# Optimization experiments

Hardware: AMD Instinct MI355X
Metric: run time of the kernel (lower is better)

Reference implementation:

```python
import jax, jax.numpy as jnp
import numpy as np

K = 40        # nearest neighbors
BN_EPS = 1e-5  # nn.BatchNorm1d default eps


def _bn(x, g, b):
    # training-mode BatchNorm1d: batch mean, biased variance
    mu = x.mean(0)
    var = x.var(0)
    return g * (x - mu) / jnp.sqrt(var + BN_EPS) + b


def setup_inputs() -> dict:
    key = jax.random.key(0)
    ks = jax.random.split(key, 16)
    N, Cin, D, S, P = 8192, 16, 32, 3, 32

    def w(k, i, o):
        return jax.random.normal(k, (i, o), jnp.float32) * (1.0 / np.sqrt(i))

    return {
        "x": jax.random.normal(ks[0], (N, Cin), jnp.float32),
        "original_coords": jax.random.normal(ks[1], (N, 3), jnp.float32),
        "batch": jnp.zeros((N,), jnp.int32),
        "step_count": 0,
        "num_layer": 1,
        # pre_gravnet MLP
        "pre_w1": w(ks[2], Cin, D), "pre_b1": jnp.zeros((D,), jnp.float32),
        "pre_w2": w(ks[3], D, D), "pre_b2": jnp.zeros((D,), jnp.float32),
        "bn1_g": jnp.ones((D,), jnp.float32), "bn1_b": jnp.zeros((D,), jnp.float32),
        # GravNetConv projections
        "lin_s_w": w(ks[4], D, S),
        "lin_h_w": w(ks[5], D, P), "lin_h_b": jnp.zeros((P,), jnp.float32),
        "lin_w": w(ks[6], D + 2 * P, D), "lin_b": jnp.zeros((D,), jnp.float32),
        # post_gravnet MLP (in = out_channels + space_dims + d_shape = 32+3+32)
        "post_w1": w(ks[7], D + S + D, D), "post_b1": jnp.zeros((D,), jnp.float32),
        "post_w2": w(ks[8], D, D), "post_b2": jnp.zeros((D,), jnp.float32),
        "bn2_g": jnp.ones((D,), jnp.float32), "bn2_b": jnp.zeros((D,), jnp.float32),
    }


def reference(x, original_coords, batch, step_count, num_layer,
              pre_w1, pre_b1, pre_w2, pre_b2, bn1_g, bn1_b,
              lin_s_w, lin_h_w, lin_h_b, lin_w, lin_b,
              post_w1, post_b1, post_w2, post_b2, bn2_g, bn2_b):
    N = x.shape[0]

    # pre_gravnet MLP + batchnorm
    h = jax.nn.elu(x @ pre_w1 + pre_b1)
    h = jax.nn.elu(h @ pre_w2 + pre_b2)
    x_in = _bn(h, bn1_g, bn1_b)

    # GravNetConv projections
    h_l = x_in @ lin_h_w + lin_h_b          # [N, P] propagated features
    s_l = x_in @ lin_s_w                    # [N, S] learned coordinate space

    # kNN graph in s-space (self loops excluded)
    sq = jnp.sum(s_l * s_l, axis=1)
    d2 = sq[:, None] + sq[None, :] - 2.0 * (s_l @ s_l.T)   # [N, N]
    d2 = jnp.maximum(d2, 0.0)
    d2 = jnp.where(jnp.eye(N, dtype=bool), jnp.inf, d2)
    _, idx = jax.lax.top_k(-d2, K)           # [N, K] neighbor indices

    # per-edge squared distance (NOTE: propagate uses the SQUARED distance,
    # faithful to the source where edge_weight is never re-bound to sqrt)
    edge_sq = jnp.take_along_axis(d2, idx, axis=1)    # [N, K]
    dist = jnp.sqrt(edge_sq + 1e-6)                   # [N, K]

    # DGL-side reductions at dst = edge_index[1] = neighbor index
    dst = idx.reshape(-1)
    distf = dist.reshape(-1)
    indeg = jax.ops.segment_sum(jnp.ones_like(distf), dst, num_segments=N)
    sum_d = jax.ops.segment_sum(distf, dst, num_segments=N)
    avdist = jnp.where(indeg > 0, sum_d / jnp.maximum(indeg, 1.0), 0.0)
    loss_regularizing_neig = 0.01 * jnp.mean(jnp.square(avdist - 0.5))

    norm_d = distf / (sum_d + 1e-4)[dst]              # EdgeWeightNorm('right')
    # faithful to source bug: '_edge_w_gndist' is set to the NORMALIZED dist,
    # and apply_edges multiplies by the RAW '_edge_w'
    degs2 = jax.ops.segment_sum(norm_d, dst, num_segments=N) + 1e-4
    gn_final = distf / degs2[dst]
    loss_llregulariser = 0.1 * jnp.mean(jnp.square(norm_d - gn_final))

    # message passing: msg = h_l[neighbor] * squared_dist, mean+max over the
    # K neighbors of each source node (regular fan-in -> dense reduce)
    msgs = h_l[idx] * edge_sq[..., None]              # [N, K, P]
    agg = jnp.concatenate([msgs.mean(1), msgs.max(1)], axis=-1)  # [N, 2P]
    xgn = jnp.concatenate([agg, x_in], axis=-1) @ lin_w + lin_b   # [N, 32]

    # post_gravnet MLP + batchnorm
    cat = jnp.concatenate([xgn, s_l, x_in], axis=1)   # [N, 67]
    o = jax.nn.elu(cat @ post_w1 + post_b1)
    o = jax.nn.elu(o @ post_w2 + post_b2)
    out = _bn(o, bn2_g, bn2_b)
    return (out, loss_regularizing_neig, loss_llregulariser)
```

## Files before the change

### kernel.cpp

```cpp
#include <hip/hip_runtime.h>
#include <math.h>

#define NPTS 8192
#define KNN 40
#define DD 32
#define CIN 16
#define RPB 8
#define QT 1024
#define NQTR (NPTS / QT)
#define KQPB 16
#define CAP 96

#define OFF_H      0u
#define OFF_XIN    262144u
#define OFF_HL     524288u
#define OFF_SL     786432u
#define OFF_ESQ    819200u
#define OFF_O      1146880u
#define OFF_IDX    1409024u
#define OFF_SUMD   1736704u
#define OFF_INDEG  1744896u
#define OFF_STATS  1753088u
#define ZERO_FLOATS (8192u + 8192u + 130u * 32u)

#define ST(i) stats[(i) * 32]

__device__ __forceinline__ float elu_f(float x) { return x > 0.f ? x : (expf(x) - 1.f); }

__device__ __forceinline__ float grp_sum32(float v) {
#pragma unroll
    for (int m = 1; m < 32; m <<= 1) v += __shfl_xor(v, m);
    return v;
}

__device__ __forceinline__ float rfl(float v) {
    return __int_as_float(__builtin_amdgcn_readfirstlane(__float_as_int(v)));
}

__device__ __forceinline__ unsigned fkey(float x) {
    unsigned b = __float_as_uint(x);
    return b ^ ((unsigned)((int)b >> 31) | 0x80000000u);
}
__device__ __forceinline__ float kinv(unsigned k) {
    unsigned b = (k & 0x80000000u) ? (k ^ 0x80000000u) : ~k;
    return __uint_as_float(b);
}

__device__ __forceinline__ unsigned bisect_kth(unsigned u0, unsigned u1, int kth) {
    unsigned lo = 0u, hi = 0xFFFFFFFFu;
    while (lo < hi) {
        unsigned mid = lo + ((hi - lo) >> 1);
        int cnt = __popcll(__ballot(u0 <= mid)) + __popcll(__ballot(u1 <= mid));
        if (cnt >= kth) hi = mid; else lo = mid + 1;
    }
    return hi;
}

__global__ __launch_bounds__(256) void k_pre(const float* __restrict__ x,
    const float* __restrict__ w1, const float* __restrict__ b1,
    const float* __restrict__ w2, const float* __restrict__ b2,
    float* __restrict__ h, float* __restrict__ stats)
{
    __shared__ float sw1[CIN * DD], sw2[DD * DD], sb1[DD], sb2[DD];
    __shared__ float bufx[RPB][20], buft[RPB][36];
    __shared__ float sstat[2 * DD];
    int tid = threadIdx.x;
    for (int t = tid; t < CIN * DD; t += 256) sw1[t] = w1[t];
    for (int t = tid; t < DD * DD; t += 256) sw2[t] = w2[t];
    if (tid < DD) { sb1[tid] = b1[tid]; sb2[tid] = b2[tid]; }
    if (tid < 2 * DD) sstat[tid] = 0.f;

    int r = tid >> 5, ch = tid & 31;
    int g = blockIdx.x * RPB + r;
    if (ch < CIN) bufx[r][ch] = x[(size_t)g * CIN + ch];
    __syncthreads();

    float acc = sb1[ch];
#pragma unroll
    for (int k4 = 0; k4 < CIN; k4 += 4) {
        float4 v = *(const float4*)&bufx[r][k4];
        acc = fmaf(v.x, sw1[(k4 + 0) * DD + ch], acc);
        acc = fmaf(v.y, sw1[(k4 + 1) * DD + ch], acc);
        acc = fmaf(v.z, sw1[(k4 + 2) * DD + ch], acc);
        acc = fmaf(v.w, sw1[(k4 + 3) * DD + ch], acc);
    }
    acc = elu_f(acc);
    buft[r][ch] = acc;
    __syncthreads();

    float o = sb2[ch];
#pragma unroll
    for (int k4 = 0; k4 < DD; k4 += 4) {
        float4 v = *(const float4*)&buft[r][k4];
        o = fmaf(v.x, sw2[(k4 + 0) * DD + ch], o);
        o = fmaf(v.y, sw2[(k4 + 1) * DD + ch], o);
        o = fmaf(v.z, sw2[(k4 + 2) * DD + ch], o);
        o = fmaf(v.w, sw2[(k4 + 3) * DD + ch], o);
    }
    o = elu_f(o);
    h[(size_t)g * DD + ch] = o;

    float s = o + __shfl_xor(o, 32);
    float q = o * o;
    q += __shfl_xor(q, 32);
    if ((tid & 32) == 0) { atomicAdd(&sstat[ch], s); atomicAdd(&sstat[DD + ch], q); }
    __syncthreads();
    if (tid < 2 * DD) atomicAdd(&ST(tid), sstat[tid]);
}

__global__ __launch_bounds__(256) void k_proj(const float* __restrict__ h,
    const float* __restrict__ stats,
    const float* __restrict__ g1, const float* __restrict__ b1g,
    const float* __restrict__ hw, const float* __restrict__ hb,
    const float* __restrict__ sw,
    float* __restrict__ xin, float* __restrict__ hl, float4* __restrict__ sl4)
{
    __shared__ float shw[DD * DD], ssw[DD * 3], sa[DD], sbp[DD], shb[DD];
    __shared__ float rrow[RPB][36];
    int tid = threadIdx.x;
    for (int t = tid; t < DD * DD; t += 256) shw[t] = hw[t];
    if (tid < DD * 3) ssw[tid] = sw[tid];
    if (tid < DD) {
        float mean = ST(tid) * (1.f / NPTS);
        float var = ST(32 + tid) * (1.f / NPTS) - mean * mean;
        float a = g1[tid] * rsqrtf(var + 1e-5f);
        sa[tid] = a;
        sbp[tid] = b1g[tid] - a * mean;
        shb[tid] = hb[tid];
    }
    __syncthreads();

    int r = tid >> 5, ch = tid & 31;
    int g = blockIdx.x * RPB + r;

    float v = fmaf(sa[ch], h[(size_t)g * DD + ch], sbp[ch]);
    xin[(size_t)g * DD + ch] = v;
    rrow[r][ch] = v;

    float p0 = v * ssw[ch * 3 + 0];
    float p1 = v * ssw[ch * 3 + 1];
    float p2 = v * ssw[ch * 3 + 2];
    p0 = grp_sum32(p0); p1 = grp_sum32(p1); p2 = grp_sum32(p2);
    if (ch == 0) sl4[g] = make_float4(p0, p1, p2, 0.5f * (p0 * p0 + p1 * p1 + p2 * p2));
    __syncthreads();

    float o = shb[ch];
#pragma unroll
    for (int k4 = 0; k4 < DD; k4 += 4) {
        float4 vv = *(const float4*)&rrow[r][k4];
        o = fmaf(vv.x, shw[(k4 + 0) * DD + ch], o);
        o = fmaf(vv.y, shw[(k4 + 1) * DD + ch], o);
        o = fmaf(vv.z, shw[(k4 + 2) * DD + ch], o);
        o = fmaf(vv.w, shw[(k4 + 3) * DD + ch], o);
    }
    hl[(size_t)g * DD + ch] = o;
}

__device__ __forceinline__ void select_emit(const float2* bufq, int C, int qidx,
    float qw, int lane, int* __restrict__ idxo, float* __restrict__ esq,
    float* __restrict__ sumd, float* __restrict__ indeg)
{
    float e0 = INFINITY, e1 = INFINITY;
    int j0 = -1, j1 = -1;
    if (lane < C) { float2 t = bufq[lane]; e0 = t.x; j0 = __float_as_int(t.y); }
    if (lane + 64 < C) { float2 t = bufq[lane + 64]; e1 = t.x; j1 = __float_as_int(t.y); }
    if (j0 == qidx) e0 = INFINITY;
    if (j1 == qidx) e1 = INFINITY;
    unsigned u0 = fkey(e0), u1 = fkey(e1);
    unsigned thr = bisect_kth(u0, u1, KNN);
    unsigned long long ltm = (1ull << lane) - 1;
    unsigned long long mlt0 = __ballot(u0 < thr), mlt1 = __ballot(u1 < thr);
    unsigned long long meq0 = __ballot(u0 == thr), meq1 = __ballot(u1 == thr);
    int nlt = __popcll(mlt0) + __popcll(mlt1);
    int need = KNN - nlt;
    int rb = qidx * KNN;

    int pos = -1;
    if (u0 < thr) pos = __popcll(mlt0 & ltm);
    else if (u0 == thr) { int rk = __popcll(meq0 & ltm); if (rk < need) pos = nlt + rk; }
    if (pos >= 0) {
        float d2 = fmaxf(2.f * (e0 + qw), 0.f);
        idxo[rb + pos] = j0; esq[rb + pos] = d2;
        float dist = sqrtf(d2 + 1e-6f);
        atomicAdd(&sumd[j0], dist); atomicAdd(&indeg[j0], 1.f);
    }
    pos = -1;
    if (u1 < thr) pos = __popcll(mlt0) + __popcll(mlt1 & ltm);
    else if (u1 == thr) {
        int rk = __popcll(meq0) + __popcll(meq1 & ltm);
        if (rk < need) pos = nlt + rk;
    }
    if (pos >= 0) {
        float d2 = fmaxf(2.f * (e1 + qw), 0.f);
        idxo[rb + pos] = j1; esq[rb + pos] = d2;
        float dist = sqrtf(d2 + 1e-6f);
        atomicAdd(&sumd[j1], dist); atomicAdd(&indeg[j1], 1.f);
    }
}

typedef __attribute__((address_space(1))) const unsigned glds_src_t;
typedef __attribute__((address_space(3))) unsigned glds_dst_t;

__global__ __launch_bounds__(512, 6) void k_knn(const float4* __restrict__ sl4,
    int* __restrict__ idxo, float* __restrict__ esq,
    float* __restrict__ sumd, float* __restrict__ indeg)
{
    __shared__ float4 tile[2][QT];
    __shared__ float2 cand[KQPB][CAP];
    int tid = threadIdx.x, lane = tid & 63, w = tid >> 6;
    int qbase = blockIdx.x * KQPB;
    int qai = qbase + 2 * w, qbi = qai + 1;
    float4 qa4 = sl4[qai], qb4 = sl4[qbi];
    float qax = rfl(qa4.x), qay = rfl(qa4.y), qaz = rfl(qa4.z);
    float qbx = rfl(qb4.x), qby = rfl(qb4.y), qbz = rfl(qb4.z);

#define STAGE(qt, b) { \
    _Pragma("unroll") \
    for (int c = 0; c < 2; ++c) { \
        int off = w * 128 + c * 64; \
        __builtin_amdgcn_global_load_lds( \
            (glds_src_t*)(sl4 + (qt) * QT + off + lane), \
            (glds_dst_t*)&tile[b][off], 16, 0, 0); \
    } }

#define EDQ(p, ex, ey, ez) fmaf(-(ex), (p).x, fmaf(-(ey), (p).y, fmaf(-(ez), (p).z, (p).w)))

    float m0a = INFINITY, m1a = INFINITY, m0b = INFINITY, m1b = INFINITY;
    STAGE(0, 0)
    __syncthreads();
    for (int t = 0; t < NQTR; ++t) {
        if (t + 1 < NQTR) STAGE(t + 1, (t + 1) & 1)
        const float4* tp = tile[t & 1];
#pragma unroll 4
        for (int i = 0; i < QT / 64; ++i) {
            float4 p = tp[i * 64 + lane];
            float ea = EDQ(p, qax, qay, qaz);
            float eb = EDQ(p, qbx, qby, qbz);
            float lo = fminf(ea, m0a), hi = fmaxf(ea, m0a);
            m0a = lo; m1a = fminf(m1a, hi);
            lo = fminf(eb, m0b); hi = fmaxf(eb, m0b);
            m0b = lo; m1b = fminf(m1b, hi);
        }
        __syncthreads();
    }
    float thra = kinv(bisect_kth(fkey(m0a), fkey(m1a), KNN + 1));
    float thrb = kinv(bisect_kth(fkey(m0b), fkey(m1b), KNN + 1));

    unsigned long long ltm = (1ull << lane) - 1;
    int ca = 0, cb = 0;
    float2* bufa = cand[2 * w];
    float2* bufb = cand[2 * w + 1];

#define COLL(e, thrv, cnt, brow, jj) { \
        unsigned long long mm = __ballot((e) <= (thrv)); \
        if (mm) { \
            if ((e) <= (thrv)) { \
                int pos = cnt + __popcll(mm & ltm); \
                if (pos < CAP) brow[pos] = make_float2((e), __int_as_float(jj)); \
            } \
            cnt += __popcll(mm); \
        } }

    STAGE(0, 0)
    __syncthreads();
    for (int t = 0; t < NQTR; ++t) {
        if (t + 1 < NQTR) STAGE(t + 1, (t + 1) & 1)
        const float4* tp = tile[t & 1];
        int tb = t * QT;
#pragma unroll 4
        for (int i = 0; i < QT / 64; ++i) {
            float4 p = tp[i * 64 + lane];
            int jj = tb + i * 64 + lane;
            float ea = EDQ(p, qax, qay, qaz);
            float eb = EDQ(p, qbx, qby, qbz);
            COLL(ea, thra, ca, bufa, jj)
            COLL(eb, thrb, cb, bufb, jj)
        }
        __syncthreads();
    }

    select_emit(bufa, ca < CAP ? ca : CAP, qai, rfl(qa4.w), lane, idxo, esq, sumd, indeg);
    select_emit(bufb, cb < CAP ? cb : CAP, qbi, rfl(qb4.w), lane, idxo, esq, sumd, indeg);
}

__global__ __launch_bounds__(256) void k_agg(
    const int* __restrict__ idx, const float* __restrict__ esq,
    const float* __restrict__ hl, const float* __restrict__ xin,
    const float4* __restrict__ sl4,
    const float* __restrict__ sumd, const float* __restrict__ indeg,
    const float* __restrict__ lw, const float* __restrict__ lb,
    const float* __restrict__ pw1, const float* __restrict__ pb1,
    const float* __restrict__ pw2, const float* __restrict__ pb2,
    float* __restrict__ o, float* __restrict__ stats)
{
    __shared__ float slw[96 * DD], spw1[67 * DD], spw2[DD * DD];
    __shared__ float slb[DD], spb1[DD], spb2[DD];
    __shared__ float rbuf[RPB][100];
    __shared__ float rb2[RPB][68];
    __shared__ float sstat[2 * DD];
    __shared__ float sl1, sl2;
    int tid = threadIdx.x;
    for (int t = tid; t < 96 * DD; t += 256) slw[t] = lw[t];
    for (int t = tid; t < 67 * DD; t += 256) spw1[t] = pw1[t];
    for (int t = tid; t < DD * DD; t += 256) spw2[t] = pw2[t];
    if (tid < DD) { slb[tid] = lb[tid]; spb1[tid] = pb1[tid]; spb2[tid] = pb2[tid]; }
    if (tid < 2 * DD) sstat[tid] = 0.f;
    if (tid == 254) sl1 = 0.f;
    if (tid == 255) sl2 = 0.f;

    int r = tid >> 5, ch = tid & 31;
    int g = blockIdx.x * RPB + r;
    int rb = g * KNN;
    int half = tid & 32;

    int   idx_c = idx[rb + ch];
    float esq_c = esq[rb + ch];
    int   idx_h = 0; float esq_h = 0.f;
    if (ch < KNN - 32) { idx_h = idx[rb + 32 + ch]; esq_h = esq[rb + 32 + ch]; }

    float sv = 0.f, mv = -INFINITY;
#pragma unroll
    for (int k = 0; k < KNN; ++k) {
        int j   = (k < 32) ? __shfl(idx_c, half | k) : __shfl(idx_h, half | (k - 32));
        float w = (k < 32) ? __shfl(esq_c, half | k) : __shfl(esq_h, half | (k - 32));
        float m = hl[(size_t)j * DD + ch] * w;
        sv += m;
        mv = fmaxf(mv, m);
    }
    rbuf[r][ch] = sv * (1.f / KNN);
    rbuf[r][32 + ch] = mv;
    rbuf[r][64 + ch] = xin[(size_t)g * DD + ch];
    if (ch == 0) { float4 s = sl4[g]; rbuf[r][96] = s.x; rbuf[r][97] = s.y; rbuf[r][98] = s.z; }
    __syncthreads();

    float l2 = 0.f;
    {
        float dist = sqrtf(esq_c + 1e-6f);
        float sd = sumd[idx_c];
        float r1 = 1.f / (sd + 1e-4f);
        float dg = sd * r1 + 1e-4f;
        float df = dist * r1 - dist / dg;
        l2 = df * df;
        if (ch < KNN - 32) {
            dist = sqrtf(esq_h + 1e-6f);
            sd = sumd[idx_h];
            r1 = 1.f / (sd + 1e-4f);
            dg = sd * r1 + 1e-4f;
            df = dist * r1 - dist / dg;
            l2 += df * df;
        }
    }
    l2 = grp_sum32(l2);
    if (ch == 0) {
        float id = indeg[g], sdg = sumd[g];
        float av = id > 0.f ? sdg / fmaxf(id, 1.f) : 0.f;
        float dd = av - 0.5f;
        atomicAdd(&sl2, l2);
        atomicAdd(&sl1, dd * dd);
    }

    float acc = slb[ch];
#pragma unroll
    for (int k4 = 0; k4 < 96; k4 += 4) {
        float4 v = *(const float4*)&rbuf[r][k4];
        acc = fmaf(v.x, slw[(k4 + 0) * DD + ch], acc);
        acc = fmaf(v.y, slw[(k4 + 1) * DD + ch], acc);
        acc = fmaf(v.z, slw[(k4 + 2) * DD + ch], acc);
        acc = fmaf(v.w, slw[(k4 + 3) * DD + ch], acc);
    }
    rb2[r][ch] = acc;
    __syncthreads();

    acc = spb1[ch];
#pragma unroll
    for (int k4 = 0; k4 < DD; k4 += 4) {
        float4 v = *(const float4*)&rb2[r][k4];
        acc = fmaf(v.x, spw1[(k4 + 0) * DD + ch], acc);
        acc = fmaf(v.y, spw1[(k4 + 1) * DD + ch], acc);
        acc = fmaf(v.z, spw1[(k4 + 2) * DD + ch], acc);
        acc = fmaf(v.w, spw1[(k4 + 3) * DD + ch], acc);
    }
#pragma unroll
    for (int s2 = 0; s2 < 3; ++s2)
        acc = fmaf(rbuf[r][96 + s2], spw1[(32 + s2) * DD + ch], acc);
#pragma unroll
    for (int k4 = 0; k4 < DD; k4 += 4) {
        float4 v = *(const float4*)&rbuf[r][64 + k4];
        acc = fmaf(v.x, spw1[(35 + k4 + 0) * DD + ch], acc);
        acc = fmaf(v.y, spw1[(35 + k4 + 1) * DD + ch], acc);
        acc = fmaf(v.z, spw1[(35 + k4 + 2) * DD + ch], acc);
        acc = fmaf(v.w, spw1[(35 + k4 + 3) * DD + ch], acc);
    }
    acc = elu_f(acc);
    rb2[r][32 + ch] = acc;
    __syncthreads();

    acc = spb2[ch];
#pragma unroll
    for (int k4 = 0; k4 < DD; k4 += 4) {
        float4 v = *(const float4*)&rb2[r][32 + k4];
        acc = fmaf(v.x, spw2[(k4 + 0) * DD + ch], acc);
        acc = fmaf(v.y, spw2[(k4 + 1) * DD + ch], acc);
        acc = fmaf(v.z, spw2[(k4 + 2) * DD + ch], acc);
        acc = fmaf(v.w, spw2[(k4 + 3) * DD + ch], acc);
    }
    acc = elu_f(acc);
    o[(size_t)g * DD + ch] = acc;

    float s = acc + __shfl_xor(acc, 32);
    float q = acc * acc;
    q += __shfl_xor(q, 32);
    if ((tid & 32) == 0) { atomicAdd(&sstat[ch], s); atomicAdd(&sstat[DD + ch], q); }
    __syncthreads();
    if (tid < 2 * DD) atomicAdd(&ST(64 + tid), sstat[tid]);
    if (tid == 0) { atomicAdd(&ST(128), sl1); atomicAdd(&ST(129), sl2); }
}

__global__ __launch_bounds__(256) void k_out(const float* __restrict__ o,
    const float* __restrict__ stats, const float* __restrict__ g,
    const float* __restrict__ b, float* __restrict__ dout)
{
    __shared__ float sa[DD], sb[DD];
    int tid = threadIdx.x;
    if (tid < DD) {
        float mean = ST(64 + tid) * (1.f / NPTS);
        float var = ST(96 + tid) * (1.f / NPTS) - mean * mean;
        float a = g[tid] * rsqrtf(var + 1e-5f);
        sa[tid] = a;
        sb[tid] = b[tid] - a * mean;
    }
    __syncthreads();

    int t = blockIdx.x * 256 + tid;
    float4 v = ((const float4*)o)[t];
    int cbase = (t * 4) & (DD - 1);
    float4 rr;
    rr.x = fmaf(sa[cbase + 0], v.x, sb[cbase + 0]);
    rr.y = fmaf(sa[cbase + 1], v.y, sb[cbase + 1]);
    rr.z = fmaf(sa[cbase + 2], v.z, sb[cbase + 2]);
    rr.w = fmaf(sa[cbase + 3], v.w, sb[cbase + 3]);
    ((float4*)dout)[t] = rr;

    if (blockIdx.x == 0) {
        if (tid == DD)     dout[NPTS * DD]     = 0.01f * ST(128) * (1.f / NPTS);
        if (tid == DD + 1) dout[NPTS * DD + 1] = 0.1f  * ST(129) * (1.f / ((float)NPTS * KNN));
    }
}

extern "C" void kernel_launch(void* const* d_in, const int* in_sizes, int n_in,
                              void* d_out, int out_size, void* d_ws, size_t ws_size,
                              hipStream_t stream)
{
    (void)in_sizes; (void)n_in; (void)out_size; (void)ws_size;
    const float* x      = (const float*)d_in[0];
    const float* pre_w1 = (const float*)d_in[5];
    const float* pre_b1 = (const float*)d_in[6];
    const float* pre_w2 = (const float*)d_in[7];
    const float* pre_b2 = (const float*)d_in[8];
    const float* bn1_g  = (const float*)d_in[9];
    const float* bn1_b  = (const float*)d_in[10];
    const float* lin_s_w = (const float*)d_in[11];
    const float* lin_h_w = (const float*)d_in[12];
    const float* lin_h_b = (const float*)d_in[13];
    const float* lin_w   = (const float*)d_in[14];
    const float* lin_b   = (const float*)d_in[15];
    const float* post_w1 = (const float*)d_in[16];
    const float* post_b1 = (const float*)d_in[17];
    const float* post_w2 = (const float*)d_in[18];
    const float* post_b2 = (const float*)d_in[19];
    const float* bn2_g   = (const float*)d_in[20];
    const float* bn2_b   = (const float*)d_in[21];

    float* W = (float*)d_ws;
    float* h     = W + OFF_H;
    float* xin   = W + OFF_XIN;
    float* hl    = W + OFF_HL;
    float4* sl4  = (float4*)(W + OFF_SL);
    float* esq   = W + OFF_ESQ;
    float* o     = W + OFF_O;
    int*   idx   = (int*)(W + OFF_IDX);
    float* sumd  = W + OFF_SUMD;
    float* indeg = W + OFF_INDEG;
    float* stats = W + OFF_STATS;
    float* dout  = (float*)d_out;

    hipMemsetAsync(W + OFF_SUMD, 0, ZERO_FLOATS * sizeof(float), stream);

    k_pre<<<NPTS / RPB, 256, 0, stream>>>(x, pre_w1, pre_b1, pre_w2, pre_b2, h, stats);
    k_proj<<<NPTS / RPB, 256, 0, stream>>>(h, stats, bn1_g, bn1_b,
                                           lin_h_w, lin_h_b, lin_s_w, xin, hl, sl4);
    k_knn<<<NPTS / KQPB, 512, 0, stream>>>(sl4, idx, esq, sumd, indeg);
    k_agg<<<NPTS / RPB, 256, 0, stream>>>(idx, esq, hl, xin, sl4, sumd, indeg,
                                          lin_w, lin_b, post_w1, post_b1, post_w2, post_b2,
                                          o, stats);
    k_out<<<NPTS * DD / 1024, 256, 0, stream>>>(o, stats, bn2_g, bn2_b, dout);
}
```

Baseline: 120.6 us.

## Replace two-pass kNN with single-pass per-lane top-4 and fallback insertion

The kNN kernel switches from two passes over all points (first finding a per-lane top-2 threshold, then collecting candidates into shared memory) to a single pass. In that pass each lane keeps its 4 smallest distances plus a 5th-smallest sentinel. A wave-wide bisection then picks the 40 nearest from the 256 per-lane candidates, and an exact check confirms no lane's unkept 5th candidate could belong in the set. If the check fails, a slow serial insertion-sort fallback rescans all points. The kernel also goes from two queries per wave to one, which doubles the grid size, and drops the shared candidate buffer. This roughly halves the distance-evaluation work per query, at the cost of more registers, per-element branching, and occasional slow fallbacks.

```diff
diff --git a/kernel.cpp b/kernel.cpp
--- a/kernel.cpp
+++ b/kernel.cpp
@@ -7,9 +7,7 @@
 #define CIN 16
 #define RPB 8
 #define QT 1024
-#define NQTR (NPTS / QT)
-#define KQPB 16
-#define CAP 96
+#define NT8 (NPTS / QT)
 
 #define OFF_H      0u
 #define OFF_XIN    262144u
@@ -46,11 +44,13 @@
     return __uint_as_float(b);
 }
 
-__device__ __forceinline__ unsigned bisect_kth(unsigned u0, unsigned u1, int kth) {
+__device__ __forceinline__ unsigned bisect_kth4(unsigned u0, unsigned u1,
+    unsigned u2, unsigned u3, int kth) {
     unsigned lo = 0u, hi = 0xFFFFFFFFu;
     while (lo < hi) {
         unsigned mid = lo + ((hi - lo) >> 1);
-        int cnt = __popcll(__ballot(u0 <= mid)) + __popcll(__ballot(u1 <= mid));
+        int cnt = __popcll(__ballot(u0 <= mid)) + __popcll(__ballot(u1 <= mid))
+                + __popcll(__ballot(u2 <= mid)) + __popcll(__ballot(u3 <= mid));
         if (cnt >= kth) hi = mid; else lo = mid + 1;
     }
     return hi;
@@ -156,131 +156,155 @@
     hl[(size_t)g * DD + ch] = o;
 }
 
-__device__ __forceinline__ void select_emit(const float2* bufq, int C, int qidx,
-    float qw, int lane, int* __restrict__ idxo, float* __restrict__ esq,
+__device__ __forceinline__ void emit_one(unsigned u, int j, float qw,
+    unsigned thr, int nlt, int need, int prelt, int preeq,
+    unsigned long long mlt, unsigned long long meq, unsigned long long ltm,
+    int rb, int* __restrict__ idxo, float* __restrict__ esq,
     float* __restrict__ sumd, float* __restrict__ indeg)
 {
-    float e0 = INFINITY, e1 = INFINITY;
-    int j0 = -1, j1 = -1;
-    if (lane < C) { float2 t = bufq[lane]; e0 = t.x; j0 = __float_as_int(t.y); }
-    if (lane + 64 < C) { float2 t = bufq[lane + 64]; e1 = t.x; j1 = __float_as_int(t.y); }
-    if (j0 == qidx) e0 = INFINITY;
-    if (j1 == qidx) e1 = INFINITY;
-    unsigned u0 = fkey(e0), u1 = fkey(e1);
-    unsigned thr = bisect_kth(u0, u1, KNN);
-    unsigned long long ltm = (1ull << lane) - 1;
-    unsigned long long mlt0 = __ballot(u0 < thr), mlt1 = __ballot(u1 < thr);
-    unsigned long long meq0 = __ballot(u0 == thr), meq1 = __ballot(u1 == thr);
-    int nlt = __popcll(mlt0) + __popcll(mlt1);
-    int need = KNN - nlt;
-    int rb = qidx * KNN;
-
     int pos = -1;
-    if (u0 < thr) pos = __popcll(mlt0 & ltm);
-    else if (u0 == thr) { int rk = __popcll(meq0 & ltm); if (rk < need) pos = nlt + rk; }
+    if (u < thr) pos = prelt + __popcll(mlt & ltm);
+    else if (u == thr) {
+        int rk = preeq + __popcll(meq & ltm);
+        if (rk < need) pos = nlt + rk;
+    }
     if (pos >= 0) {
-        float d2 = fmaxf(2.f * (e0 + qw), 0.f);
-        idxo[rb + pos] = j0; esq[rb + pos] = d2;
+        float e = kinv(u);
+        float d2 = fmaxf(2.f * (e + qw), 0.f);
+        idxo[rb + pos] = j; esq[rb + pos] = d2;
         float dist = sqrtf(d2 + 1e-6f);
-        atomicAdd(&sumd[j0], dist); atomicAdd(&indeg[j0], 1.f);
-    }
-    pos = -1;
-    if (u1 < thr) pos = __popcll(mlt0) + __popcll(mlt1 & ltm);
-    else if (u1 == thr) {
-        int rk = __popcll(meq0) + __popcll(meq1 & ltm);
-        if (rk < need) pos = nlt + rk;
-    }
-    if (pos >= 0) {
-        float d2 = fmaxf(2.f * (e1 + qw), 0.f);
-        idxo[rb + pos] = j1; esq[rb + pos] = d2;
-        float dist = sqrtf(d2 + 1e-6f);
-        atomicAdd(&sumd[j1], dist); atomicAdd(&indeg[j1], 1.f);
+        atomicAdd(&sumd[j], dist); atomicAdd(&indeg[j], 1.f);
     }
 }
 
 typedef __attribute__((address_space(1))) const unsigned glds_src_t;
 typedef __attribute__((address_space(3))) unsigned glds_dst_t;
 
-__global__ __launch_bounds__(512, 6) void k_knn(const float4* __restrict__ sl4,
+#define EDQ(p, ex, ey, ez) fmaf(-(ex), (p).x, fmaf(-(ey), (p).y, fmaf(-(ez), (p).z, (p).w)))
+
+__device__ void knn_fallback(const float4* __restrict__ sl4, int qi,
+    float qx, float qy, float qz, float qw_, int lane,
     int* __restrict__ idxo, float* __restrict__ esq,
     float* __restrict__ sumd, float* __restrict__ indeg)
 {
+    float h_d = INFINITY;
+    int   h_i = 0;
+    float gate = INFINITY;
+
+    for (int base = 0; base < NPTS; base += 64) {
+        int j = base + lane;
+        float4 p = sl4[j];
+        float e = EDQ(p, qx, qy, qz);
+        if (j == qi) e = INFINITY;
+        unsigned long long m = __ballot(e < gate);
+        while (m) {
+            int src = __ffsll(m) - 1;
+            m &= m - 1;
+            float db = __shfl(e, src);
+            if (db < gate) {
+                unsigned long long pm = __ballot(db < h_d) & 0xFFFFFFFFFFull;
+                if (pm) {
+                    int jb = base + src;
+                    int pos = __ffsll(pm) - 1;
+                    float sh = __shfl_up(h_d, 1);
+                    int   si = __shfl_up(h_i, 1);
+                    bool seg = (lane > pos) && (lane < KNN);
+                    h_d = (lane == pos) ? db : (seg ? sh : h_d);
+                    h_i = (lane == pos) ? jb : (seg ? si : h_i);
+                    gate = __shfl(h_d, KNN - 1);
+                }
+            }
+        }
+    }
+    if (lane < KNN) {
+        int rb = qi * KNN + lane;
+        float d2 = fmaxf(2.f * (h_d + qw_), 0.f);
+        idxo[rb] = h_i;
+        esq[rb] = d2;
+        float dist = sqrtf(d2 + 1e-6f);
+        atomicAdd(&sumd[h_i], dist);
+        atomicAdd(&indeg[h_i], 1.f);
+    }
+}
+
+__global__ __launch_bounds__(512, 8) void k_knn(const float4* __restrict__ sl4,
+    int* __restrict__ idxo, float* __restrict__ esq,
+    float* __restrict__ sumd, float* __restrict__ indeg)
+{
     __shared__ float4 tile[2][QT];
-    __shared__ float2 cand[KQPB][CAP];
     int tid = threadIdx.x, lane = tid & 63, w = tid >> 6;
-    int qbase = blockIdx.x * KQPB;
-    int qai = qbase + 2 * w, qbi = qai + 1;
-    float4 qa4 = sl4[qai], qb4 = sl4[qbi];
-    float qax = rfl(qa4.x), qay = rfl(qa4.y), qaz = rfl(qa4.z);
-    float qbx = rfl(qb4.x), qby = rfl(qb4.y), qbz = rfl(qb4.z);
-
-#define STAGE(qt, b) { \
+    int qi = blockIdx.x * 8 + w;
+    float4 q4 = sl4[qi];
+    float qx = rfl(q4.x), qy = rfl(q4.y), qz = rfl(q4.z), qw_ = rfl(q4.w);
+
+#define STAGE(t, b) { \
     _Pragma("unroll") \
     for (int c = 0; c < 2; ++c) { \
         int off = w * 128 + c * 64; \
         __builtin_amdgcn_global_load_lds( \
-            (glds_src_t*)(sl4 + (qt) * QT + off + lane), \
+            (glds_src_t*)(sl4 + (t) * QT + off + lane), \
             (glds_dst_t*)&tile[b][off], 16, 0, 0); \
     } }
 
-#define EDQ(p, ex, ey, ez) fmaf(-(ex), (p).x, fmaf(-(ey), (p).y, fmaf(-(ez), (p).z, (p).w)))
-
-    float m0a = INFINITY, m1a = INFINITY, m0b = INFINITY, m1b = INFINITY;
+    float e0 = INFINITY, e1 = INFINITY, e2 = INFINITY, e3 = INFINITY, e5 = INFINITY;
+    int j0 = -1, j1 = -1, j2 = -1, j3 = -1;
+
     STAGE(0, 0)
     __syncthreads();
-    for (int t = 0; t < NQTR; ++t) {
-        if (t + 1 < NQTR) STAGE(t + 1, (t + 1) & 1)
-        const float4* tp = tile[t & 1];
-#pragma unroll 4
-        for (int i = 0; i < QT / 64; ++i) {
-            float4 p = tp[i * 64 + lane];
-            float ea = EDQ(p, qax, qay, qaz);
-            float eb = EDQ(p, qbx, qby, qbz);
-            float lo = fminf(ea, m0a), hi = fmaxf(ea, m0a);
-            m0a = lo; m1a = fminf(m1a, hi);
-            lo = fminf(eb, m0b); hi = fmaxf(eb, m0b);
-            m0b = lo; m1b = fminf(m1b, hi);
-        }
-        __syncthreads();
-    }
-    float thra = kinv(bisect_kth(fkey(m0a), fkey(m1a), KNN + 1));
-    float thrb = kinv(bisect_kth(fkey(m0b), fkey(m1b), KNN + 1));
-
-    unsigned long long ltm = (1ull << lane) - 1;
-    int ca = 0, cb = 0;
-    float2* bufa = cand[2 * w];
-    float2* bufb = cand[2 * w + 1];
-
-#define COLL(e, thrv, cnt, brow, jj) { \
-        unsigned long long mm = __ballot((e) <= (thrv)); \
-        if (mm) { \
-            if ((e) <= (thrv)) { \
-                int pos = cnt + __popcll(mm & ltm); \
-                if (pos < CAP) brow[pos] = make_float2((e), __int_as_float(jj)); \
-            } \
-            cnt += __popcll(mm); \
-        } }
-
-    STAGE(0, 0)
-    __syncthreads();
-    for (int t = 0; t < NQTR; ++t) {
-        if (t + 1 < NQTR) STAGE(t + 1, (t + 1) & 1)
+    for (int t = 0; t < NT8; ++t) {
+        if (t + 1 < NT8) STAGE(t + 1, (t + 1) & 1)
         const float4* tp = tile[t & 1];
         int tb = t * QT;
 #pragma unroll 4
         for (int i = 0; i < QT / 64; ++i) {
             float4 p = tp[i * 64 + lane];
-            int jj = tb + i * 64 + lane;
-            float ea = EDQ(p, qax, qay, qaz);
-            float eb = EDQ(p, qbx, qby, qbz);
-            COLL(ea, thra, ca, bufa, jj)
-            COLL(eb, thrb, cb, bufb, jj)
+            float e = EDQ(p, qx, qy, qz);
+            e5 = fminf(e5, fmaxf(e, e3));
+            if (e < e3) {
+                e3 = e; j3 = tb + i * 64 + lane;
+                if (e3 < e2) {
+                    float tv = e2; e2 = e3; e3 = tv;
+                    int tj = j2; j2 = j3; j3 = tj;
+                    if (e2 < e1) {
+                        tv = e1; e1 = e2; e2 = tv;
+                        tj = j1; j1 = j2; j2 = tj;
+                        if (e1 < e0) {
+                            tv = e0; e0 = e1; e1 = tv;
+                            tj = j0; j0 = j1; j1 = tj;
+                        }
+                    }
+                }
+            }
         }
         __syncthreads();
     }
 
-    select_emit(bufa, ca < CAP ? ca : CAP, qai, rfl(qa4.w), lane, idxo, esq, sumd, indeg);
-    select_emit(bufb, cb < CAP ? cb : CAP, qbi, rfl(qb4.w), lane, idxo, esq, sumd, indeg);
+    float f0 = (j0 == qi) ? INFINITY : e0;
+    float f1 = (j1 == qi) ? INFINITY : e1;
+    float f2 = (j2 == qi) ? INFINITY : e2;
+    float f3 = (j3 == qi) ? INFINITY : e3;
+    unsigned u0 = fkey(f0), u1 = fkey(f1), u2 = fkey(f2), u3 = fkey(f3);
+    unsigned thr = bisect_kth4(u0, u1, u2, u3, KNN);
+
+    bool miss = __ballot(fkey(e5) <= thr) != 0ull;
+    if (!miss) {
+        unsigned long long ltm = (1ull << lane) - 1;
+        unsigned long long mlt0 = __ballot(u0 < thr), mlt1 = __ballot(u1 < thr);
+        unsigned long long mlt2 = __ballot(u2 < thr), mlt3 = __ballot(u3 < thr);
+        unsigned long long meq0 = __ballot(u0 == thr), meq1 = __ballot(u1 == thr);
+        unsigned long long meq2 = __ballot(u2 == thr), meq3 = __ballot(u3 == thr);
+        int n0 = __popcll(mlt0), n1 = __popcll(mlt1), n2 = __popcll(mlt2), n3 = __popcll(mlt3);
+        int q0c = __popcll(meq0), q1c = __popcll(meq1), q2c = __popcll(meq2);
+        int nlt = n0 + n1 + n2 + n3;
+        int need = KNN - nlt;
+        int rb = qi * KNN;
+        emit_one(u0, j0, qw_, thr, nlt, need, 0, 0, mlt0, meq0, ltm, rb, idxo, esq, sumd, indeg);
+        emit_one(u1, j1, qw_, thr, nlt, need, n0, q0c, mlt1, meq1, ltm, rb, idxo, esq, sumd, indeg);
+        emit_one(u2, j2, qw_, thr, nlt, need, n0 + n1, q0c + q1c, mlt2, meq2, ltm, rb, idxo, esq, sumd, indeg);
+        emit_one(u3, j3, qw_, thr, nlt, need, n0 + n1 + n2, q0c + q1c + q2c, mlt3, meq3, ltm, rb, idxo, esq, sumd, indeg);
+    } else {
+        knn_fallback(sl4, qi, qx, qy, qz, qw_, lane, idxo, esq, sumd, indeg);
+    }
 }
 
 __global__ __launch_bounds__(256) void k_agg(
@@ -489,7 +513,7 @@
     k_pre<<<NPTS / RPB, 256, 0, stream>>>(x, pre_w1, pre_b1, pre_w2, pre_b2, h, stats);
     k_proj<<<NPTS / RPB, 256, 0, stream>>>(h, stats, bn1_g, bn1_b,
                                            lin_h_w, lin_h_b, lin_s_w, xin, hl, sl4);
-    k_knn<<<NPTS / KQPB, 512, 0, stream>>>(sl4, idx, esq, sumd, indeg);
+    k_knn<<<NPTS / 8, 512, 0, stream>>>(sl4, idx, esq, sumd, indeg);
     k_agg<<<NPTS / RPB, 256, 0, stream>>>(idx, esq, hl, xin, sl4, sumd, indeg,
                                           lin_w, lin_b, post_w1, post_b1, post_w2, post_b2,
                                           o, stats);
```

New measurement: 181.3 us. +50.3%, slower.
